# Optimization experiments

Hardware: AMD Instinct MI355X
Metric: run time of the kernel (lower is better)

The kernel has to match this reference:

```python
import jax, jax.numpy as jnp
import numpy as np

T, N, F = 8, 4096, 128
LPF, HPF, H, LP_HID, E = 128, 128, 256, 256, 131072
D = LPF + HPF


def setup_inputs() -> dict:
    key = jax.random.key(0)
    ks = jax.random.split(key, 16)
    s = lambda k, *shape: jax.random.normal(k, shape, dtype=jnp.float32) * 0.05
    feats = jax.random.normal(ks[0], (T, N, F), dtype=jnp.float32)
    # row-stochastic-ish propagation matrices
    p = jax.random.uniform(ks[1], (T, N, N), dtype=jnp.float32)
    p = p / jnp.sum(p, axis=-1, keepdims=True)
    eidx = jax.random.randint(ks[2], (2, E), 0, N, dtype=jnp.int64)
    return {
        "features": feats,
        "p_matrix": p,
        "predict_edge_index": eidx,
        "W_lpf": s(ks[3], F, LPF), "b_lpf": jnp.zeros((LPF,), jnp.float32),
        "W_hpf": s(ks[4], F, HPF), "b_hpf": jnp.zeros((HPF,), jnp.float32),
        "W_ih": s(ks[5], 4 * H, D), "W_hh": s(ks[6], 4 * H, H),
        "b_ih": jnp.zeros((4 * H,), jnp.float32), "b_hh": jnp.zeros((4 * H,), jnp.float32),
        "W1": s(ks[7], 2 * H, LP_HID), "b1": jnp.zeros((LP_HID,), jnp.float32),
        "W2": s(ks[8], LP_HID, 1), "b2": jnp.zeros((1,), jnp.float32),
    }


def reference(features, p_matrix, predict_edge_index, W_lpf, b_lpf, W_hpf, b_hpf,
              W_ih, W_hh, b_ih, b_hh, W1, b1, W2, b2):
    # --- batched low/high-pass graph filters over all T snapshots ---
    xw = jnp.einsum('tnf,fd->tnd', features, W_lpf)          # X @ W_lp
    low = jax.nn.relu(jnp.einsum('tnm,tmd->tnd', p_matrix, xw) + b_lpf)
    px = jnp.einsum('tnm,tmf->tnf', p_matrix, features)      # P @ X
    high = jax.nn.relu(jnp.einsum('tnf,fd->tnd', features - px, W_hpf) + b_hpf)
    x_seq = jnp.concatenate([low, high], axis=-1)            # [T, N, D]

    # --- LSTM over time, nodes as batch (torch gate order i,f,g,o) ---
    def step(carry, x_t):
        h, c = carry
        gates = x_t @ W_ih.T + h @ W_hh.T + (b_ih + b_hh)    # [N, 4H]
        i, f, g, o = jnp.split(gates, 4, axis=-1)
        c = jax.nn.sigmoid(f) * c + jax.nn.sigmoid(i) * jnp.tanh(g)
        h = jax.nn.sigmoid(o) * jnp.tanh(c)
        return (h, c), None

    h0 = jnp.zeros((N, H), x_seq.dtype)
    (h_fin, _), _ = jax.lax.scan(step, (h0, h0), x_seq)      # final timestep hidden

    # --- gather + concat + MLP link predictor ---
    src = h_fin[predict_edge_index[0]]
    dst = h_fin[predict_edge_index[1]]
    comb = jnp.concatenate([src, dst], axis=-1)              # [E, 2H]
    hid = jax.nn.relu(comb @ W1 + b1)
    logits = (hid @ W2 + b2).squeeze(-1)                     # [E]
    return logits
```

## Files before the change

### kernel.cpp

```cpp
#include <hip/hip_runtime.h>
#include <stdint.h>

#define T_ 8
#define N_ 4096
#define E_ 131072

typedef __attribute__((ext_vector_type(4))) float f32x4;
typedef __attribute__((ext_vector_type(8))) short s16x8;
typedef __attribute__((ext_vector_type(4))) short s16x4;

static __device__ __forceinline__ short f2bf(float f) {
    union { float f; unsigned u; } v; v.f = f;
    unsigned r = v.u + 0x7fffu + ((v.u >> 16) & 1u);
    return (short)(r >> 16);
}
static __device__ __forceinline__ float bf2f(short s) {
    union { float f; unsigned u; } v; v.u = ((unsigned)(unsigned short)s) << 16;
    return v.f;
}

static __device__ __forceinline__ void bar_nodrain() {
    asm volatile("s_waitcnt lgkmcnt(0)\n\ts_barrier" ::: "memory");
}

__global__ __launch_bounds__(256) void pack_yt(const float* __restrict__ feat,
                                               short* __restrict__ yt) {
    __shared__ float tile[32][33];
    const int t = blockIdx.z, j0 = blockIdx.y * 32, n0 = blockIdx.x * 32;
    const float* src = feat + (size_t)t * N_ * 128 + j0;
    const int jj = threadIdx.x & 31, i4 = threadIdx.x >> 5;
#pragma unroll
    for (int s = 0; s < 4; s++) {
        int ii = i4 * 4 + s;
        tile[ii][jj] = src[(size_t)(n0 + ii) * 128 + jj];
    }
    __syncthreads();
    const int nn = threadIdx.x & 31, j4 = threadIdx.x >> 5;
#pragma unroll
    for (int s = 0; s < 4; s++) {
        int j2 = j4 * 4 + s;
        yt[(size_t)(t * 128 + j0 + j2) * N_ + n0 + nn] = f2bf(tile[nn][j2]);
    }
}

__global__ __launch_bounds__(512) void pfy_gemm(const float* __restrict__ P,
                                                const short* __restrict__ Yt,
                                                float* __restrict__ Z) {
    __shared__ short As[2][128][72];
    __shared__ short Bs[2][128][72];
    const int t = blockIdx.y;
    const int m0 = blockIdx.x * 128;
    const int tid = threadIdx.x;
    const int lane = tid & 63, wid = tid >> 6;
    const int wm = wid >> 2, wn = wid & 3;
    const int frow = lane & 15, kq = lane >> 4;

    const float* Pt = P + (size_t)t * N_ * N_;
    const short* Bt = Yt + (size_t)t * 128 * N_;

    const int ar = tid >> 2;
    const int ak16 = (tid & 3) * 16;
    const int bj = tid >> 2;
    const int bk16 = (tid & 3) * 16;

    f32x4 acc[4][2];
    f32x4 zf = {0.f, 0.f, 0.f, 0.f};
#pragma unroll
    for (int m = 0; m < 4; m++)
#pragma unroll
        for (int n = 0; n < 2; n++) acc[m][n] = zf;

    f32x4 aA[4], aB[4]; s16x8 bA[2], bB[2];

    const float* Pr = &Pt[(size_t)(m0 + ar) * 4096 + ak16];
    const short* Br = &Bt[(size_t)bj * 4096 + bk16];

#define LOADA(KT) do { const int k0_ = (KT) * 64;                              \
        _Pragma("unroll") for (int i = 0; i < 4; i++)                          \
            aA[i] = *(const f32x4*)&Pr[k0_ + i * 4];                           \
        _Pragma("unroll") for (int i = 0; i < 2; i++)                          \
            bA[i] = *(const s16x8*)&Br[k0_ + i * 8]; } while (0)
#define LOADB(KT) do { const int k0_ = (KT) * 64;                              \
        _Pragma("unroll") for (int i = 0; i < 4; i++)                          \
            aB[i] = *(const f32x4*)&Pr[k0_ + i * 4];                           \
        _Pragma("unroll") for (int i = 0; i < 2; i++)                          \
            bB[i] = *(const s16x8*)&Br[k0_ + i * 8]; } while (0)
#define STOREA(BUF) do {                                                       \
        _Pragma("unroll") for (int i = 0; i < 4; i++) {                        \
            s16x4 c4_;                                                         \
            _Pragma("unroll") for (int j = 0; j < 4; j++) c4_[j] = f2bf(aA[i][j]); \
            *(s16x4*)&As[BUF][ar][ak16 + i * 4] = c4_; }                       \
        _Pragma("unroll") for (int i = 0; i < 2; i++)                          \
            *(s16x8*)&Bs[BUF][bj][bk16 + i * 8] = bA[i]; } while (0)
#define STOREB(BUF) do {                                                       \
        _Pragma("unroll") for (int i = 0; i < 4; i++) {                        \
            s16x4 c4_;                                                         \
            _Pragma("unroll") for (int j = 0; j < 4; j++) c4_[j] = f2bf(aB[i][j]); \
            *(s16x4*)&As[BUF][ar][ak16 + i * 4] = c4_; }                       \
        _Pragma("unroll") for (int i = 0; i < 2; i++)                          \
            *(s16x8*)&Bs[BUF][bj][bk16 + i * 8] = bB[i]; } while (0)

    auto compute_t = [&](int buf) {
#pragma unroll
        for (int ks = 0; ks < 2; ks++) {
            s16x8 af[4], bfr[2];
#pragma unroll
            for (int m = 0; m < 4; m++)
                af[m] = *(const s16x8*)&As[buf][wm * 64 + m * 16 + frow][kq * 8 + ks * 32];
#pragma unroll
            for (int n = 0; n < 2; n++)
                bfr[n] = *(const s16x8*)&Bs[buf][wn * 32 + n * 16 + frow][kq * 8 + ks * 32];
#pragma unroll
            for (int m = 0; m < 4; m++)
#pragma unroll
                for (int n = 0; n < 2; n++)
                    acc[m][n] = __builtin_amdgcn_mfma_f32_16x16x32_bf16(af[m], bfr[n], acc[m][n], 0, 0, 0);
        }
    };

    LOADA(0);
    STOREA(0);
    LOADB(1);
    LOADA(2);
    bar_nodrain();

#pragma unroll 2
    for (int kt = 0; kt < 64; kt++) {
        compute_t(kt & 1);
        if (kt < 63) {
            if ((kt & 1) == 0) {
                STOREB(1);
                if (kt + 3 < 64) LOADB(kt + 3);
            } else {
                STOREA(0);
                if (kt + 3 < 64) LOADA(kt + 3);
            }
            bar_nodrain();
        }
    }
#undef LOADA
#undef LOADB
#undef STOREA
#undef STOREB

    float* Zt = Z + (size_t)t * N_ * 128;
#pragma unroll
    for (int m = 0; m < 4; m++)
#pragma unroll
        for (int n = 0; n < 2; n++)
#pragma unroll
            for (int r = 0; r < 4; r++) {
                int row = m0 + wm * 64 + m * 16 + kq * 4 + r;
                int col = wn * 32 + n * 16 + frow;
                Zt[(size_t)row * 128 + col] = acc[m][n][r];
            }
}

__global__ __launch_bounds__(256) void hp2_gemm(const float* __restrict__ feat,
                                                const float* __restrict__ PX,
                                                const float* __restrict__ Wlp,
                                                const float* __restrict__ Whp,
                                                const float* __restrict__ b_lpf,
                                                const float* __restrict__ b_hpf,
                                                short* __restrict__ xhi,
                                                short* __restrict__ xlo) {
    __shared__ float As[32][68];
    __shared__ float Ws[32][132];
    const int m0 = blockIdx.x * 64;
    const int mode = blockIdx.y;
    const float* W = mode ? Whp : Wlp;
    const float* bp = mode ? b_hpf : b_lpf;
    const int tid = threadIdx.x;
    const int rg = tid & 15, cg = tid >> 4;
    float acc[4][8];
#pragma unroll
    for (int r = 0; r < 4; r++)
#pragma unroll
        for (int c = 0; c < 8; c++) acc[r][c] = 0.f;

    for (int k0 = 0; k0 < 128; k0 += 32) {
#pragma unroll
        for (int s = 0; s < 2; s++) {
            int q = tid + s * 256, row = q >> 3, k4 = q & 7;
            f32x4 pv = *(const f32x4*)&PX[(size_t)(m0 + row) * 128 + k0 + k4 * 4];
            f32x4 v;
            if (mode) {
                f32x4 fv = *(const f32x4*)&feat[(size_t)(m0 + row) * 128 + k0 + k4 * 4];
#pragma unroll
                for (int i = 0; i < 4; i++) v[i] = fv[i] - pv[i];
            } else {
                v = pv;
            }
#pragma unroll
            for (int i = 0; i < 4; i++) As[k4 * 4 + i][row] = v[i];
        }
#pragma unroll
        for (int s = 0; s < 4; s++) {
            int q = tid + s * 256, kk = q >> 5, j4 = q & 31;
            *(f32x4*)&Ws[kk][j4 * 4] = *(const f32x4*)&W[(size_t)(k0 + kk) * 128 + j4 * 4];
        }
        __syncthreads();
#pragma unroll
        for (int kk = 0; kk < 32; kk++) {
            f32x4 a  = *(const f32x4*)&As[kk][rg * 4];
            f32x4 w0 = *(const f32x4*)&Ws[kk][cg * 8];
            f32x4 w1 = *(const f32x4*)&Ws[kk][cg * 8 + 4];
#pragma unroll
            for (int r = 0; r < 4; r++)
#pragma unroll
                for (int c = 0; c < 4; c++) {
                    acc[r][c]     += a[r] * w0[c];
                    acc[r][c + 4] += a[r] * w1[c];
                }
        }
        __syncthreads();
    }
    float bh[8];
#pragma unroll
    for (int c = 0; c < 8; c++) bh[c] = bp[cg * 8 + c];
#pragma unroll
    for (int r = 0; r < 4; r++) {
        s16x4 h0, h1, l0, l1;
#pragma unroll
        for (int c = 0; c < 4; c++) {
            float v0 = fmaxf(acc[r][c] + bh[c], 0.f);
            float v1 = fmaxf(acc[r][c + 4] + bh[c + 4], 0.f);
            h0[c] = f2bf(v0); l0[c] = f2bf(v0 - bf2f(h0[c]));
            h1[c] = f2bf(v1); l1[c] = f2bf(v1 - bf2f(h1[c]));
        }
        size_t base = (size_t)(m0 + rg * 4 + r) * 256 + mode * 128 + cg * 8;
        *(s16x4*)&xhi[base] = h0;  *(s16x4*)&xhi[base + 4] = h1;
        *(s16x4*)&xlo[base] = l0;  *(s16x4*)&xlo[base + 4] = l1;
    }
}

__global__ __launch_bounds__(256) void pack_wc(const float* __restrict__ W_ih,
                                               const float* __restrict__ W_hh,
                                               short* __restrict__ whi,
                                               short* __restrict__ wlo) {
    int idx = (blockIdx.x * 256 + threadIdx.x) * 4;
    int j = idx >> 9, k = idx & 511;
    int orig = (j & 3) * 256 + (j >> 2);
    const float* src = (k < 256) ? &W_ih[(size_t)orig * 256 + k]
                                 : &W_hh[(size_t)orig * 256 + (k - 256)];
    f32x4 v = *(const f32x4*)src;
    s16x4 hi, lo;
#pragma unroll
    for (int i = 0; i < 4; i++) {
        hi[i] = f2bf(v[i]);
        lo[i] = f2bf(v[i] - bf2f(hi[i]));
    }
    *(s16x4*)&whi[idx] = hi;
    *(s16x4*)&wlo[idx] = lo;
}

__global__ void pack_bias(const float* __restrict__ b_ih,
                          const float* __restrict__ b_hh,
                          float* __restrict__ bsum) {
    int j = blockIdx.x * 256 + threadIdx.x;
    int orig = (j & 3) * 256 + (j >> 2);
    bsum[j] = b_ih[orig] + b_hh[orig];
}

__global__ __launch_bounds__(512) void lstm_step(const short* __restrict__ xhi,
                                                 const short* __restrict__ xlo,
                                                 const short* __restrict__ hhi_r,
                                                 const short* __restrict__ hlo_r,
                                                 const short* __restrict__ wchi,
                                                 const short* __restrict__ wclo,
                                                 const float* __restrict__ bsum,
                                                 float* __restrict__ cbuf,
                                                 short* __restrict__ hhi_w,
                                                 short* __restrict__ hlo_w) {
    __shared__ short Ah[2][128][40], Al[2][128][40];
    __shared__ short Bh[2][128][40], Bl[2][128][40];
    __shared__ float gl[128][132];
    const int m0 = blockIdx.x * 128;
    const int j0 = blockIdx.y * 128;
    const int tid = threadIdx.x;
    const int lane = tid & 63, wid = tid >> 6;
    const int wm = wid >> 2, wn = wid & 3;
    const int frow = lane & 15, kq = lane >> 4;

    const int sr = tid >> 2;
    const int sk8 = (tid & 3) * 8;

    f32x4 acc[4][2];
    f32x4 zf = {0.f, 0.f, 0.f, 0.f};
#pragma unroll
    for (int m = 0; m < 4; m++)
#pragma unroll
        for (int n = 0; n < 2; n++) acc[m][n] = zf;

    s16x8 a_h, a_l, b_h, b_l;

    auto load_t = [&](int kt) {
        const int k0 = kt * 32;
        const short* ah = (k0 < 256) ? xhi : hhi_r;
        const short* al = (k0 < 256) ? xlo : hlo_r;
        const size_t abase = (size_t)(m0 + sr) * 256 + (k0 & 255) + sk8;
        a_h = *(const s16x8*)&ah[abase];
        a_l = *(const s16x8*)&al[abase];
        const size_t bb = (size_t)(j0 + sr) * 512 + k0 + sk8;
        b_h = *(const s16x8*)&wchi[bb];
        b_l = *(const s16x8*)&wclo[bb];
    };
    auto store_t = [&](int buf) {
        *(s16x8*)&Ah[buf][sr][sk8] = a_h;
        *(s16x8*)&Al[buf][sr][sk8] = a_l;
        *(s16x8*)&Bh[buf][sr][sk8] = b_h;
        *(s16x8*)&Bl[buf][sr][sk8] = b_l;
    };
    auto compute_t = [&](int buf) {
        s16x8 afh[4], afl[4], bfh[2], bfl[2];
#pragma unroll
        for (int m = 0; m < 4; m++) {
            afh[m] = *(const s16x8*)&Ah[buf][wm * 64 + m * 16 + frow][kq * 8];
            afl[m] = *(const s16x8*)&Al[buf][wm * 64 + m * 16 + frow][kq * 8];
        }
#pragma unroll
        for (int n = 0; n < 2; n++) {
            bfh[n] = *(const s16x8*)&Bh[buf][wn * 32 + n * 16 + frow][kq * 8];
            bfl[n] = *(const s16x8*)&Bl[buf][wn * 32 + n * 16 + frow][kq * 8];
        }
#pragma unroll
        for (int m = 0; m < 4; m++)
#pragma unroll
            for (int n = 0; n < 2; n++) {
                acc[m][n] = __builtin_amdgcn_mfma_f32_16x16x32_bf16(afh[m], bfh[n], acc[m][n], 0, 0, 0);
                acc[m][n] = __builtin_amdgcn_mfma_f32_16x16x32_bf16(afh[m], bfl[n], acc[m][n], 0, 0, 0);
                acc[m][n] = __builtin_amdgcn_mfma_f32_16x16x32_bf16(afl[m], bfh[n], acc[m][n], 0, 0, 0);
            }
    };

    load_t(0);
    store_t(0);
    bar_nodrain();
#pragma unroll 2
    for (int kt = 0; kt < 16; kt++) {
        const int cur = kt & 1;
        if (kt < 15) load_t(kt + 1);
        compute_t(cur);
        bar_nodrain();
        if (kt < 15) { store_t(cur ^ 1); bar_nodrain(); }
    }

#pragma unroll
    for (int m = 0; m < 4; m++)
#pragma unroll
        for (int n = 0; n < 2; n++)
#pragma unroll
            for (int r = 0; r < 4; r++)
                gl[wm * 64 + m * 16 + kq * 4 + r][wn * 32 + n * 16 + frow] = acc[m][n][r];
    bar_nodrain();

    const int erow = tid >> 2;
    const int ec0 = (tid & 3) * 8;
    const size_t cbase = (size_t)(m0 + erow) * 256 + blockIdx.y * 32 + ec0;
    f32x4 co0 = *(const f32x4*)&cbuf[cbase];
    f32x4 co1 = *(const f32x4*)&cbuf[cbase + 4];
    f32x4 cn0, cn1;
    s16x8 h8, l8;
#pragma unroll
    for (int i = 0; i < 8; i++) {
        f32x4 g4 = *(const f32x4*)&gl[erow][(ec0 + i) * 4];
        f32x4 bs = *(const f32x4*)&bsum[j0 + (ec0 + i) * 4];
        float si = 1.f / (1.f + expf(-(g4[0] + bs[0])));
        float sf = 1.f / (1.f + expf(-(g4[1] + bs[1])));
        float tg = tanhf(g4[2] + bs[2]);
        float so = 1.f / (1.f + expf(-(g4[3] + bs[3])));
        float cold = (i < 4) ? co0[i] : co1[i - 4];
        float cn = sf * cold + si * tg;
        float hv = so * tanhf(cn);
        if (i < 4) cn0[i] = cn; else cn1[i - 4] = cn;
        h8[i] = f2bf(hv);
        l8[i] = f2bf(hv - bf2f(h8[i]));
    }
    *(f32x4*)&cbuf[cbase] = cn0;
    *(f32x4*)&cbuf[cbase + 4] = cn1;
    *(s16x8*)&hhi_w[cbase] = h8;
    *(s16x8*)&hlo_w[cbase] = l8;
}

__global__ __launch_bounds__(256) void pack_w1c(const float* __restrict__ W1,
                                                short* __restrict__ whi,
                                                short* __restrict__ wlo) {
    __shared__ float tile[32][33];
    const int k0 = blockIdx.x * 32;
    const int j0 = blockIdx.y * 32;
    const int koff = (j0 >= 256) ? 256 : 0;
    const int joff = (j0 >= 256) ? 256 : 0;
    const int jj = threadIdx.x & 31, k4 = threadIdx.x >> 5;
#pragma unroll
    for (int s = 0; s < 4; s++) {
        int kk = k4 * 4 + s;
        tile[kk][jj] = W1[(size_t)(k0 + kk + koff) * 256 + (j0 + jj - joff)];
    }
    __syncthreads();
    const int kk2 = threadIdx.x & 31, j4 = threadIdx.x >> 5;
#pragma unroll
    for (int s = 0; s < 4; s++) {
        int j2 = j4 * 4 + s;
        float v = tile[kk2][j2];
        short hb = f2bf(v);
        whi[(size_t)(j0 + j2) * 256 + k0 + kk2] = hb;
        wlo[(size_t)(j0 + j2) * 256 + k0 + kk2] = f2bf(v - bf2f(hb));
    }
}

__global__ __launch_bounds__(512) void uv_gemm(const short* __restrict__ hhi,
                                               const short* __restrict__ hlo,
                                               const short* __restrict__ whi,
                                               const short* __restrict__ wlo,
                                               float* __restrict__ UV) {
    __shared__ short Ah[2][128][40], Al[2][128][40];
    __shared__ short Bh[2][128][40], Bl[2][128][40];
    const int m0 = blockIdx.x * 128;
    const int j0 = blockIdx.y * 128;
    const int tid = threadIdx.x;
    const int lane = tid & 63, wid = tid >> 6;
    const int wm = wid >> 2, wn = wid & 3;
    const int frow = lane & 15, kq = lane >> 4;
    const int sr = tid >> 2;
    const int sk8 = (tid & 3) * 8;

    f32x4 acc[4][2];
    f32x4 zf = {0.f, 0.f, 0.f, 0.f};
#pragma unroll
    for (int m = 0; m < 4; m++)
#pragma unroll
        for (int n = 0; n < 2; n++) acc[m][n] = zf;

    s16x8 a_h, a_l, b_h, b_l;

    auto load_t = [&](int kt) {
        const int k0 = kt * 32;
        const size_t abase = (size_t)(m0 + sr) * 256 + k0 + sk8;
        a_h = *(const s16x8*)&hhi[abase];
        a_l = *(const s16x8*)&hlo[abase];
        const size_t bb = (size_t)(j0 + sr) * 256 + k0 + sk8;
        b_h = *(const s16x8*)&whi[bb];
        b_l = *(const s16x8*)&wlo[bb];
    };
    auto store_t = [&](int buf) {
        *(s16x8*)&Ah[buf][sr][sk8] = a_h;
        *(s16x8*)&Al[buf][sr][sk8] = a_l;
        *(s16x8*)&Bh[buf][sr][sk8] = b_h;
        *(s16x8*)&Bl[buf][sr][sk8] = b_l;
    };
    auto compute_t = [&](int buf) {
        s16x8 afh[4], afl[4], bfh[2], bfl[2];
#pragma unroll
        for (int m = 0; m < 4; m++) {
            afh[m] = *(const s16x8*)&Ah[buf][wm * 64 + m * 16 + frow][kq * 8];
            afl[m] = *(const s16x8*)&Al[buf][wm * 64 + m * 16 + frow][kq * 8];
        }
#pragma unroll
        for (int n = 0; n < 2; n++) {
            bfh[n] = *(const s16x8*)&Bh[buf][wn * 32 + n * 16 + frow][kq * 8];
            bfl[n] = *(const s16x8*)&Bl[buf][wn * 32 + n * 16 + frow][kq * 8];
        }
#pragma unroll
        for (int m = 0; m < 4; m++)
#pragma unroll
            for (int n = 0; n < 2; n++) {
                acc[m][n] = __builtin_amdgcn_mfma_f32_16x16x32_bf16(afh[m], bfh[n], acc[m][n], 0, 0, 0);
                acc[m][n] = __builtin_amdgcn_mfma_f32_16x16x32_bf16(afh[m], bfl[n], acc[m][n], 0, 0, 0);
                acc[m][n] = __builtin_amdgcn_mfma_f32_16x16x32_bf16(afl[m], bfh[n], acc[m][n], 0, 0, 0);
            }
    };

    load_t(0);
    store_t(0);
    bar_nodrain();
#pragma unroll 2
    for (int kt = 0; kt < 8; kt++) {
        const int cur = kt & 1;
        if (kt < 7) load_t(kt + 1);
        compute_t(cur);
        bar_nodrain();
        if (kt < 7) { store_t(cur ^ 1); bar_nodrain(); }
    }

#pragma unroll
    for (int m = 0; m < 4; m++)
#pragma unroll
        for (int n = 0; n < 2; n++)
#pragma unroll
            for (int r = 0; r < 4; r++) {
                int row = m0 + wm * 64 + m * 16 + kq * 4 + r;
                int col = j0 + wn * 32 + n * 16 + frow;
                UV[(size_t)row * 512 + col] = acc[m][n][r];
            }
}

__global__ __launch_bounds__(256) void mlp_edge(const float* __restrict__ UV,
                                                const int* __restrict__ eidx,
                                                const float* __restrict__ b1,
                                                const float* __restrict__ W2,
                                                const float* __restrict__ b2,
                                                float* __restrict__ out) {
    const int e = blockIdx.x * 4 + (threadIdx.x >> 6);
    const int lane = threadIdx.x & 63;
    const int c4 = lane * 4;
    const int src = eidx[e];
    const int dst = eidx[E_ + e];
    f32x4 u = *(const f32x4*)&UV[(size_t)src * 512 + c4];
    f32x4 v = *(const f32x4*)&UV[(size_t)dst * 512 + 256 + c4];
    f32x4 bb = *(const f32x4*)&b1[c4];
    f32x4 ww = *(const f32x4*)&W2[c4];
    float p = 0.f;
#pragma unroll
    for (int i = 0; i < 4; i++)
        p += fmaxf(u[i] + v[i] + bb[i], 0.f) * ww[i];
    p += __shfl_xor(p, 1);
    p += __shfl_xor(p, 2);
    p += __shfl_xor(p, 4);
    p += __shfl_xor(p, 8);
    p += __shfl_xor(p, 16);
    p += __shfl_xor(p, 32);
    if (lane == 0) out[e] = p + b2[0];
}

extern "C" void kernel_launch(void* const* d_in, const int* in_sizes, int n_in,
                              void* d_out, int out_size, void* d_ws, size_t ws_size,
                              hipStream_t stream) {
    (void)in_sizes; (void)n_in; (void)out_size; (void)ws_size;
    const float* feat  = (const float*)d_in[0];
    const float* P     = (const float*)d_in[1];
    const int*   eidx  = (const int*)d_in[2];
    const float* W_lpf = (const float*)d_in[3];
    const float* b_lpf = (const float*)d_in[4];
    const float* W_hpf = (const float*)d_in[5];
    const float* b_hpf = (const float*)d_in[6];
    const float* W_ih  = (const float*)d_in[7];
    const float* W_hh  = (const float*)d_in[8];
    const float* b_ih  = (const float*)d_in[9];
    const float* b_hh  = (const float*)d_in[10];
    const float* W1    = (const float*)d_in[11];
    const float* b1    = (const float*)d_in[12];
    const float* W2    = (const float*)d_in[13];
    const float* b2    = (const float*)d_in[14];
    float* out = (float*)d_out;

    char* ws = (char*)d_ws;
    float* xw    = (float*)ws;   ws += (size_t)T_ * N_ * 128 * 4;
    char*  ytreg = ws;           ws += (size_t)T_ * 256 * N_ * 2;
    char*  Zreg  = ws;           ws += (size_t)T_ * N_ * 256 * 4;
    short* xhi   = (short*)ws;   ws += (size_t)T_ * N_ * 256 * 2;
    short* xlo   = (short*)ws;   ws += (size_t)T_ * N_ * 256 * 2;
    (void)xw;

    short* yt    = (short*)ytreg;
    float* PX    = (float*)Zreg;
    float* cbuf  = (float*)ytreg;
    short* hhi0  = (short*)(ytreg + (size_t)N_ * 256 * 4);
    short* hlo0  = hhi0 + (size_t)N_ * 256;
    short* hhi1  = hlo0 + (size_t)N_ * 256;
    short* hlo1  = hhi1 + (size_t)N_ * 256;
    short* w1chi = (short*)Zreg;
    short* w1clo = w1chi + (size_t)512 * 256;
    short* wchi  = w1clo + (size_t)512 * 256;
    short* wclo  = wchi + (size_t)1024 * 512;
    float* bsum  = (float*)(wclo + (size_t)1024 * 512);
    float* UV    = bsum + 1024;

    pack_yt<<<dim3(N_ / 32, 4, T_), 256, 0, stream>>>(feat, yt);
    pfy_gemm<<<dim3(N_ / 128, T_), 512, 0, stream>>>(P, yt, PX);
    hp2_gemm<<<dim3(T_ * N_ / 64, 2), 256, 0, stream>>>(feat, PX, W_lpf, W_hpf,
                                                        b_lpf, b_hpf, xhi, xlo);

    pack_w1c<<<dim3(8, 16), 256, 0, stream>>>(W1, w1chi, w1clo);
    pack_wc<<<dim3(1024 * 512 / 1024), 256, 0, stream>>>(W_ih, W_hh, wchi, wclo);
    pack_bias<<<dim3(4), 256, 0, stream>>>(b_ih, b_hh, bsum);

    hipMemsetAsync(ytreg, 0, (size_t)N_ * 256 * 4 + (size_t)N_ * 256 * 2 * 2, stream);

    for (int t = 0; t < T_; t++) {
        const short* hr_hi = (t & 1) ? hhi1 : hhi0;
        const short* hr_lo = (t & 1) ? hlo1 : hlo0;
        short* hw_hi = (t & 1) ? hhi0 : hhi1;
        short* hw_lo = (t & 1) ? hlo0 : hlo1;
        lstm_step<<<dim3(N_ / 128, 1024 / 128), 512, 0, stream>>>(
            xhi + (size_t)t * N_ * 256, xlo + (size_t)t * N_ * 256,
            hr_hi, hr_lo, wchi, wclo, bsum, cbuf, hw_hi, hw_lo);
    }

    uv_gemm<<<dim3(N_ / 128, 512 / 128), 512, 0, stream>>>(hhi0, hlo0, w1chi, w1clo, UV);
    mlp_edge<<<dim3(E_ / 4), 256, 0, stream>>>(UV, eidx, b1, W2, b2, out);
}
```

Baseline: 407.5 us.

## Fuse LSTM timesteps into one cooperative persistent kernel with register-resident cell state

Replaces the eight per-timestep lstm_step launches with a single cooperative kernel that loops over time and uses grid-wide sync between steps. The cell state now stays in registers instead of a global buffer, biases are loaded once, and step 0 skips the h@W_hh half of the K loop because h is zero. The three weight/bias packing kernels are merged into one launch and the memset is removed. In exchange, correctness depends on all 256 blocks being co-resident for the grid sync, and each grid barrier has its own cost.

```diff
diff --git a/kernel.cpp b/kernel.cpp
--- a/kernel.cpp
+++ b/kernel.cpp
@@ -1,5 +1,8 @@
 #include <hip/hip_runtime.h>
+#include <hip/hip_cooperative_groups.h>
 #include <stdint.h>
+
+namespace cg = cooperative_groups;
 
 #define T_ 8
 #define N_ 4096
@@ -171,7 +174,7 @@
     const float* W = mode ? Whp : Wlp;
     const float* bp = mode ? b_hpf : b_lpf;
     const int tid = threadIdx.x;
-    const int rg = tid & 15, cg = tid >> 4;
+    const int rg = tid & 15, cg2 = tid >> 4;
     float acc[4][8];
 #pragma unroll
     for (int r = 0; r < 4; r++)
@@ -203,8 +206,8 @@
 #pragma unroll
         for (int kk = 0; kk < 32; kk++) {
             f32x4 a  = *(const f32x4*)&As[kk][rg * 4];
-            f32x4 w0 = *(const f32x4*)&Ws[kk][cg * 8];
-            f32x4 w1 = *(const f32x4*)&Ws[kk][cg * 8 + 4];
+            f32x4 w0 = *(const f32x4*)&Ws[kk][cg2 * 8];
+            f32x4 w1 = *(const f32x4*)&Ws[kk][cg2 * 8 + 4];
 #pragma unroll
             for (int r = 0; r < 4; r++)
 #pragma unroll
@@ -217,7 +220,7 @@
     }
     float bh[8];
 #pragma unroll
-    for (int c = 0; c < 8; c++) bh[c] = bp[cg * 8 + c];
+    for (int c = 0; c < 8; c++) bh[c] = bp[cg2 * 8 + c];
 #pragma unroll
     for (int r = 0; r < 4; r++) {
         s16x4 h0, h1, l0, l1;
@@ -228,50 +231,81 @@
             h0[c] = f2bf(v0); l0[c] = f2bf(v0 - bf2f(h0[c]));
             h1[c] = f2bf(v1); l1[c] = f2bf(v1 - bf2f(h1[c]));
         }
-        size_t base = (size_t)(m0 + rg * 4 + r) * 256 + mode * 128 + cg * 8;
+        size_t base = (size_t)(m0 + rg * 4 + r) * 256 + mode * 128 + cg2 * 8;
         *(s16x4*)&xhi[base] = h0;  *(s16x4*)&xhi[base + 4] = h1;
         *(s16x4*)&xlo[base] = l0;  *(s16x4*)&xlo[base + 4] = l1;
     }
 }
 
-__global__ __launch_bounds__(256) void pack_wc(const float* __restrict__ W_ih,
-                                               const float* __restrict__ W_hh,
-                                               short* __restrict__ whi,
-                                               short* __restrict__ wlo) {
-    int idx = (blockIdx.x * 256 + threadIdx.x) * 4;
-    int j = idx >> 9, k = idx & 511;
-    int orig = (j & 3) * 256 + (j >> 2);
-    const float* src = (k < 256) ? &W_ih[(size_t)orig * 256 + k]
-                                 : &W_hh[(size_t)orig * 256 + (k - 256)];
-    f32x4 v = *(const f32x4*)src;
-    s16x4 hi, lo;
-#pragma unroll
-    for (int i = 0; i < 4; i++) {
-        hi[i] = f2bf(v[i]);
-        lo[i] = f2bf(v[i] - bf2f(hi[i]));
-    }
-    *(s16x4*)&whi[idx] = hi;
-    *(s16x4*)&wlo[idx] = lo;
-}
-
-__global__ void pack_bias(const float* __restrict__ b_ih,
-                          const float* __restrict__ b_hh,
-                          float* __restrict__ bsum) {
-    int j = blockIdx.x * 256 + threadIdx.x;
-    int orig = (j & 3) * 256 + (j >> 2);
-    bsum[j] = b_ih[orig] + b_hh[orig];
-}
-
-__global__ __launch_bounds__(512) void lstm_step(const short* __restrict__ xhi,
-                                                 const short* __restrict__ xlo,
-                                                 const short* __restrict__ hhi_r,
-                                                 const short* __restrict__ hlo_r,
-                                                 const short* __restrict__ wchi,
-                                                 const short* __restrict__ wclo,
-                                                 const float* __restrict__ bsum,
-                                                 float* __restrict__ cbuf,
-                                                 short* __restrict__ hhi_w,
-                                                 short* __restrict__ hlo_w) {
+__global__ __launch_bounds__(256) void pack_all(const float* __restrict__ W1,
+                                                const float* __restrict__ W_ih,
+                                                const float* __restrict__ W_hh,
+                                                const float* __restrict__ b_ih,
+                                                const float* __restrict__ b_hh,
+                                                short* __restrict__ w1chi,
+                                                short* __restrict__ w1clo,
+                                                short* __restrict__ wchi,
+                                                short* __restrict__ wclo,
+                                                float* __restrict__ bsum) {
+    __shared__ float tile[32][33];
+    const int b = blockIdx.x;
+    if (b < 512) {
+        int idx = (b * 256 + threadIdx.x) * 4;
+        int j = idx >> 9, k = idx & 511;
+        int orig = (j & 3) * 256 + (j >> 2);
+        const float* src = (k < 256) ? &W_ih[(size_t)orig * 256 + k]
+                                     : &W_hh[(size_t)orig * 256 + (k - 256)];
+        f32x4 v = *(const f32x4*)src;
+        s16x4 hi, lo;
+#pragma unroll
+        for (int i = 0; i < 4; i++) {
+            hi[i] = f2bf(v[i]);
+            lo[i] = f2bf(v[i] - bf2f(hi[i]));
+        }
+        *(s16x4*)&wchi[idx] = hi;
+        *(s16x4*)&wclo[idx] = lo;
+    } else if (b < 640) {
+        const int bb = b - 512;
+        const int k0 = (bb & 7) * 32;
+        const int j0 = (bb >> 3) * 32;
+        const int koff = (j0 >= 256) ? 256 : 0;
+        const int joff = (j0 >= 256) ? 256 : 0;
+        const int jj = threadIdx.x & 31, k4 = threadIdx.x >> 5;
+#pragma unroll
+        for (int s = 0; s < 4; s++) {
+            int kk = k4 * 4 + s;
+            tile[kk][jj] = W1[(size_t)(k0 + kk + koff) * 256 + (j0 + jj - joff)];
+        }
+        __syncthreads();
+        const int kk2 = threadIdx.x & 31, j4 = threadIdx.x >> 5;
+#pragma unroll
+        for (int s = 0; s < 4; s++) {
+            int j2 = j4 * 4 + s;
+            float v = tile[kk2][j2];
+            short hb = f2bf(v);
+            w1chi[(size_t)(j0 + j2) * 256 + k0 + kk2] = hb;
+            w1clo[(size_t)(j0 + j2) * 256 + k0 + kk2] = f2bf(v - bf2f(hb));
+        }
+    } else {
+#pragma unroll
+        for (int s = 0; s < 4; s++) {
+            int j = s * 256 + threadIdx.x;
+            int orig = (j & 3) * 256 + (j >> 2);
+            bsum[j] = b_ih[orig] + b_hh[orig];
+        }
+    }
+}
+
+__global__ __launch_bounds__(512) void lstm_seq(const short* __restrict__ xhi_all,
+                                                const short* __restrict__ xlo_all,
+                                                short* __restrict__ hhi0,
+                                                short* __restrict__ hlo0,
+                                                short* __restrict__ hhi1,
+                                                short* __restrict__ hlo1,
+                                                const short* __restrict__ wchi,
+                                                const short* __restrict__ wclo,
+                                                const float* __restrict__ bsum) {
+    cg::grid_group gridg = cg::this_grid();
     __shared__ short Ah[2][128][40], Al[2][128][40];
     __shared__ short Bh[2][128][40], Bl[2][128][40];
     __shared__ float gl[128][132];
@@ -281,130 +315,116 @@
     const int lane = tid & 63, wid = tid >> 6;
     const int wm = wid >> 2, wn = wid & 3;
     const int frow = lane & 15, kq = lane >> 4;
-
     const int sr = tid >> 2;
     const int sk8 = (tid & 3) * 8;
-
-    f32x4 acc[4][2];
-    f32x4 zf = {0.f, 0.f, 0.f, 0.f};
-#pragma unroll
-    for (int m = 0; m < 4; m++)
-#pragma unroll
-        for (int n = 0; n < 2; n++) acc[m][n] = zf;
-
-    s16x8 a_h, a_l, b_h, b_l;
-
-    auto load_t = [&](int kt) {
-        const int k0 = kt * 32;
-        const short* ah = (k0 < 256) ? xhi : hhi_r;
-        const short* al = (k0 < 256) ? xlo : hlo_r;
-        const size_t abase = (size_t)(m0 + sr) * 256 + (k0 & 255) + sk8;
-        a_h = *(const s16x8*)&ah[abase];
-        a_l = *(const s16x8*)&al[abase];
-        const size_t bb = (size_t)(j0 + sr) * 512 + k0 + sk8;
-        b_h = *(const s16x8*)&wchi[bb];
-        b_l = *(const s16x8*)&wclo[bb];
-    };
-    auto store_t = [&](int buf) {
-        *(s16x8*)&Ah[buf][sr][sk8] = a_h;
-        *(s16x8*)&Al[buf][sr][sk8] = a_l;
-        *(s16x8*)&Bh[buf][sr][sk8] = b_h;
-        *(s16x8*)&Bl[buf][sr][sk8] = b_l;
-    };
-    auto compute_t = [&](int buf) {
-        s16x8 afh[4], afl[4], bfh[2], bfl[2];
-#pragma unroll
-        for (int m = 0; m < 4; m++) {
-            afh[m] = *(const s16x8*)&Ah[buf][wm * 64 + m * 16 + frow][kq * 8];
-            afl[m] = *(const s16x8*)&Al[buf][wm * 64 + m * 16 + frow][kq * 8];
-        }
-#pragma unroll
-        for (int n = 0; n < 2; n++) {
-            bfh[n] = *(const s16x8*)&Bh[buf][wn * 32 + n * 16 + frow][kq * 8];
-            bfl[n] = *(const s16x8*)&Bl[buf][wn * 32 + n * 16 + frow][kq * 8];
-        }
-#pragma unroll
-        for (int m = 0; m < 4; m++)
-#pragma unroll
-            for (int n = 0; n < 2; n++) {
-                acc[m][n] = __builtin_amdgcn_mfma_f32_16x16x32_bf16(afh[m], bfh[n], acc[m][n], 0, 0, 0);
-                acc[m][n] = __builtin_amdgcn_mfma_f32_16x16x32_bf16(afh[m], bfl[n], acc[m][n], 0, 0, 0);
-                acc[m][n] = __builtin_amdgcn_mfma_f32_16x16x32_bf16(afl[m], bfh[n], acc[m][n], 0, 0, 0);
-            }
-    };
-
-    load_t(0);
-    store_t(0);
-    bar_nodrain();
-#pragma unroll 2
-    for (int kt = 0; kt < 16; kt++) {
-        const int cur = kt & 1;
-        if (kt < 15) load_t(kt + 1);
-        compute_t(cur);
-        bar_nodrain();
-        if (kt < 15) { store_t(cur ^ 1); bar_nodrain(); }
-    }
-
-#pragma unroll
-    for (int m = 0; m < 4; m++)
-#pragma unroll
-        for (int n = 0; n < 2; n++)
-#pragma unroll
-            for (int r = 0; r < 4; r++)
-                gl[wm * 64 + m * 16 + kq * 4 + r][wn * 32 + n * 16 + frow] = acc[m][n][r];
-    bar_nodrain();
 
     const int erow = tid >> 2;
     const int ec0 = (tid & 3) * 8;
     const size_t cbase = (size_t)(m0 + erow) * 256 + blockIdx.y * 32 + ec0;
-    f32x4 co0 = *(const f32x4*)&cbuf[cbase];
-    f32x4 co1 = *(const f32x4*)&cbuf[cbase + 4];
-    f32x4 cn0, cn1;
-    s16x8 h8, l8;
-#pragma unroll
-    for (int i = 0; i < 8; i++) {
-        f32x4 g4 = *(const f32x4*)&gl[erow][(ec0 + i) * 4];
-        f32x4 bs = *(const f32x4*)&bsum[j0 + (ec0 + i) * 4];
-        float si = 1.f / (1.f + expf(-(g4[0] + bs[0])));
-        float sf = 1.f / (1.f + expf(-(g4[1] + bs[1])));
-        float tg = tanhf(g4[2] + bs[2]);
-        float so = 1.f / (1.f + expf(-(g4[3] + bs[3])));
-        float cold = (i < 4) ? co0[i] : co1[i - 4];
-        float cn = sf * cold + si * tg;
-        float hv = so * tanhf(cn);
-        if (i < 4) cn0[i] = cn; else cn1[i - 4] = cn;
-        h8[i] = f2bf(hv);
-        l8[i] = f2bf(hv - bf2f(h8[i]));
-    }
-    *(f32x4*)&cbuf[cbase] = cn0;
-    *(f32x4*)&cbuf[cbase + 4] = cn1;
-    *(s16x8*)&hhi_w[cbase] = h8;
-    *(s16x8*)&hlo_w[cbase] = l8;
-}
-
-__global__ __launch_bounds__(256) void pack_w1c(const float* __restrict__ W1,
-                                                short* __restrict__ whi,
-                                                short* __restrict__ wlo) {
-    __shared__ float tile[32][33];
-    const int k0 = blockIdx.x * 32;
-    const int j0 = blockIdx.y * 32;
-    const int koff = (j0 >= 256) ? 256 : 0;
-    const int joff = (j0 >= 256) ? 256 : 0;
-    const int jj = threadIdx.x & 31, k4 = threadIdx.x >> 5;
-#pragma unroll
-    for (int s = 0; s < 4; s++) {
-        int kk = k4 * 4 + s;
-        tile[kk][jj] = W1[(size_t)(k0 + kk + koff) * 256 + (j0 + jj - joff)];
-    }
-    __syncthreads();
-    const int kk2 = threadIdx.x & 31, j4 = threadIdx.x >> 5;
-#pragma unroll
-    for (int s = 0; s < 4; s++) {
-        int j2 = j4 * 4 + s;
-        float v = tile[kk2][j2];
-        short hb = f2bf(v);
-        whi[(size_t)(j0 + j2) * 256 + k0 + kk2] = hb;
-        wlo[(size_t)(j0 + j2) * 256 + k0 + kk2] = f2bf(v - bf2f(hb));
+    f32x4 creg0 = {0.f, 0.f, 0.f, 0.f}, creg1 = {0.f, 0.f, 0.f, 0.f};
+
+    f32x4 bs[8];
+#pragma unroll
+    for (int i = 0; i < 8; i++)
+        bs[i] = *(const f32x4*)&bsum[j0 + (ec0 + i) * 4];
+
+    for (int t = 0; t < T_; t++) {
+        const short* xhi = xhi_all + (size_t)t * N_ * 256;
+        const short* xlo = xlo_all + (size_t)t * N_ * 256;
+        const short* hr_hi = (t & 1) ? hhi1 : hhi0;
+        const short* hr_lo = (t & 1) ? hlo1 : hlo0;
+        short* hw_hi = (t & 1) ? hhi0 : hhi1;
+        short* hw_lo = (t & 1) ? hlo0 : hlo1;
+        const int nkt = (t == 0) ? 8 : 16;
+
+        f32x4 acc[4][2];
+        f32x4 zf = {0.f, 0.f, 0.f, 0.f};
+#pragma unroll
+        for (int m = 0; m < 4; m++)
+#pragma unroll
+            for (int n = 0; n < 2; n++) acc[m][n] = zf;
+
+        s16x8 a_h, a_l, b_h, b_l;
+
+        auto load_t = [&](int kt) {
+            const int k0 = kt * 32;
+            const short* ah = (k0 < 256) ? xhi : hr_hi;
+            const short* al = (k0 < 256) ? xlo : hr_lo;
+            const size_t abase = (size_t)(m0 + sr) * 256 + (k0 & 255) + sk8;
+            a_h = *(const s16x8*)&ah[abase];
+            a_l = *(const s16x8*)&al[abase];
+            const size_t bb = (size_t)(j0 + sr) * 512 + k0 + sk8;
+            b_h = *(const s16x8*)&wchi[bb];
+            b_l = *(const s16x8*)&wclo[bb];
+        };
+        auto store_t = [&](int buf) {
+            *(s16x8*)&Ah[buf][sr][sk8] = a_h;
+            *(s16x8*)&Al[buf][sr][sk8] = a_l;
+            *(s16x8*)&Bh[buf][sr][sk8] = b_h;
+            *(s16x8*)&Bl[buf][sr][sk8] = b_l;
+        };
+        auto compute_t = [&](int buf) {
+            s16x8 afh[4], afl[4], bfh[2], bfl[2];
+#pragma unroll
+            for (int m = 0; m < 4; m++) {
+                afh[m] = *(const s16x8*)&Ah[buf][wm * 64 + m * 16 + frow][kq * 8];
+                afl[m] = *(const s16x8*)&Al[buf][wm * 64 + m * 16 + frow][kq * 8];
+            }
+#pragma unroll
+            for (int n = 0; n < 2; n++) {
+                bfh[n] = *(const s16x8*)&Bh[buf][wn * 32 + n * 16 + frow][kq * 8];
+                bfl[n] = *(const s16x8*)&Bl[buf][wn * 32 + n * 16 + frow][kq * 8];
+            }
+#pragma unroll
+            for (int m = 0; m < 4; m++)
+#pragma unroll
+                for (int n = 0; n < 2; n++) {
+                    acc[m][n] = __builtin_amdgcn_mfma_f32_16x16x32_bf16(afh[m], bfh[n], acc[m][n], 0, 0, 0);
+                    acc[m][n] = __builtin_amdgcn_mfma_f32_16x16x32_bf16(afh[m], bfl[n], acc[m][n], 0, 0, 0);
+                    acc[m][n] = __builtin_amdgcn_mfma_f32_16x16x32_bf16(afl[m], bfh[n], acc[m][n], 0, 0, 0);
+                }
+        };
+
+        load_t(0);
+        store_t(0);
+        bar_nodrain();
+#pragma unroll 2
+        for (int kt = 0; kt < nkt; kt++) {
+            const int cur = kt & 1;
+            if (kt < nkt - 1) load_t(kt + 1);
+            compute_t(cur);
+            bar_nodrain();
+            if (kt < nkt - 1) { store_t(cur ^ 1); bar_nodrain(); }
+        }
+
+#pragma unroll
+        for (int m = 0; m < 4; m++)
+#pragma unroll
+            for (int n = 0; n < 2; n++)
+#pragma unroll
+                for (int r = 0; r < 4; r++)
+                    gl[wm * 64 + m * 16 + kq * 4 + r][wn * 32 + n * 16 + frow] = acc[m][n][r];
+        bar_nodrain();
+
+        s16x8 h8, l8;
+#pragma unroll
+        for (int i = 0; i < 8; i++) {
+            f32x4 g4 = *(const f32x4*)&gl[erow][(ec0 + i) * 4];
+            float si = 1.f / (1.f + expf(-(g4[0] + bs[i][0])));
+            float sf = 1.f / (1.f + expf(-(g4[1] + bs[i][1])));
+            float tg = tanhf(g4[2] + bs[i][2]);
+            float so = 1.f / (1.f + expf(-(g4[3] + bs[i][3])));
+            float cold = (i < 4) ? creg0[i] : creg1[i - 4];
+            float cn = sf * cold + si * tg;
+            float hv = so * tanhf(cn);
+            if (i < 4) creg0[i] = cn; else creg1[i - 4] = cn;
+            h8[i] = f2bf(hv);
+            l8[i] = f2bf(hv - bf2f(h8[i]));
+        }
+        *(s16x8*)&hw_hi[cbase] = h8;
+        *(s16x8*)&hw_lo[cbase] = l8;
+
+        gridg.sync();
     }
 }
 
@@ -553,8 +573,7 @@
 
     short* yt    = (short*)ytreg;
     float* PX    = (float*)Zreg;
-    float* cbuf  = (float*)ytreg;
-    short* hhi0  = (short*)(ytreg + (size_t)N_ * 256 * 4);
+    short* hhi0  = (short*)ytreg;
     short* hlo0  = hhi0 + (size_t)N_ * 256;
     short* hhi1  = hlo0 + (size_t)N_ * 256;
     short* hlo1  = hhi1 + (size_t)N_ * 256;
@@ -570,20 +589,17 @@
     hp2_gemm<<<dim3(T_ * N_ / 64, 2), 256, 0, stream>>>(feat, PX, W_lpf, W_hpf,
                                                         b_lpf, b_hpf, xhi, xlo);
 
-    pack_w1c<<<dim3(8, 16), 256, 0, stream>>>(W1, w1chi, w1clo);
-    pack_wc<<<dim3(1024 * 512 / 1024), 256, 0, stream>>>(W_ih, W_hh, wchi, wclo);
-    pack_bias<<<dim3(4), 256, 0, stream>>>(b_ih, b_hh, bsum);
-
-    hipMemsetAsync(ytreg, 0, (size_t)N_ * 256 * 4 + (size_t)N_ * 256 * 2 * 2, stream);
-
-    for (int t = 0; t < T_; t++) {
-        const short* hr_hi = (t & 1) ? hhi1 : hhi0;
-        const short* hr_lo = (t & 1) ? hlo1 : hlo0;
-        short* hw_hi = (t & 1) ? hhi0 : hhi1;
-        short* hw_lo = (t & 1) ? hlo0 : hlo1;
-        lstm_step<<<dim3(N_ / 128, 1024 / 128), 512, 0, stream>>>(
-            xhi + (size_t)t * N_ * 256, xlo + (size_t)t * N_ * 256,
-            hr_hi, hr_lo, wchi, wclo, bsum, cbuf, hw_hi, hw_lo);
+    pack_all<<<dim3(641), 256, 0, stream>>>(W1, W_ih, W_hh, b_ih, b_hh,
+                                            w1chi, w1clo, wchi, wclo, bsum);
+
+    {
+        const short* xh = xhi; const short* xl = xlo;
+        void* args[] = { (void*)&xh, (void*)&xl,
+                         (void*)&hhi0, (void*)&hlo0, (void*)&hhi1, (void*)&hlo1,
+                         (void*)&wchi, (void*)&wclo, (void*)&bsum };
+        hipLaunchCooperativeKernel(reinterpret_cast<void*>(lstm_seq),
+                                   dim3(N_ / 128, 1024 / 128), dim3(512),
+                                   args, 0, stream);
     }
 
     uv_gemm<<<dim3(N_ / 128, 512 / 128), 512, 0, stream>>>(hhi0, hlo0, w1chi, w1clo, UV);
```

Measured after the change: 651.2 us. 59.8% more time.
